# Kernel tuning notes

Hardware: AMD Instinct MI355X
Metric: run time of the kernel (lower is better)

Reference implementation:

```python
import jax, jax.numpy as jnp
import numpy as np

N_NODES = 50000
N_EDGES = 800000
D_IN = 64
D_OUT = 64


def setup_inputs() -> dict:
    key = jax.random.key(0)
    k1, k2, k3 = jax.random.split(key, 3)
    x = jax.random.normal(k1, (N_NODES, D_IN), dtype=jnp.float32)
    edge_index = jax.random.randint(k2, (2, N_EDGES), 0, N_NODES, dtype=jnp.int64)
    W = jax.random.normal(k3, (D_IN, D_OUT), dtype=jnp.float32) / np.sqrt(D_IN)
    b = jnp.zeros((D_OUT,), dtype=jnp.float32)
    return {"x": x, "edge_index": edge_index, "W": W, "b": b}


def reference(x, edge_index, W, b):
    # GCNConv with default add_self_loops=True and symmetric normalization,
    # followed by ReLU (GCN_layer activation).
    N = x.shape[0]
    loop = jnp.arange(N, dtype=edge_index.dtype)
    row = jnp.concatenate([edge_index[0], loop])  # source nodes [E+N]
    col = jnp.concatenate([edge_index[1], loop])  # target nodes [E+N]

    # degree of target nodes (includes self-loops)
    deg = jax.ops.segment_sum(jnp.ones_like(col, dtype=x.dtype), col, num_segments=N)
    deg_inv_sqrt = jnp.where(deg > 0, jax.lax.rsqrt(jnp.maximum(deg, 1.0)), 0.0)
    norm = deg_inv_sqrt[row] * deg_inv_sqrt[col]  # [E+N]

    xw = x @ W  # [N, Dout] - linear before propagation (as in PyG GCNConv)
    msg = norm[:, None] * xw[row]  # gather + per-edge scale, [E+N, Dout]
    out = jax.ops.segment_sum(msg, col, num_segments=N) + b  # scatter-add
    return jax.nn.relu(out)
```

## Files before the change

### kernel.cpp

```cpp
#include <hip/hip_runtime.h>

#define N_NODES 50000
#define N_EDGES 800000
#define D 64
#define CAP 64
#define NBLK_MM (N_NODES / 16)
#define NBLK_DEG (N_EDGES / 256)

typedef _Float16 half4_t __attribute__((ext_vector_type(4)));
typedef _Float16 half8_t __attribute__((ext_vector_type(8)));

__global__ __launch_bounds__(256) void k_mm_degbucket(const float* __restrict__ x,
                                                      const float* __restrict__ W,
                                                      _Float16* __restrict__ xwh,
                                                      const int* __restrict__ ei,
                                                      int* __restrict__ deg,
                                                      int* __restrict__ ebuf) {
    __shared__ float Wl[D * D];
    __shared__ float xl[16 * D];
    int bid = blockIdx.x >> 1;
    if (blockIdx.x & 1) {
        int e = bid * 256 + threadIdx.x;
        int r = ei[e];
        int c = ei[N_EDGES + e];
        int k = atomicAdd(&deg[c], 1);
        ebuf[(c << 6) | k] = r;
        return;
    }
    int tid = threadIdx.x;
#pragma unroll
    for (int i = tid; i < D * D / 4; i += 256)
        ((float4*)Wl)[i] = ((const float4*)W)[i];
    int r0 = bid * 16;
    ((float4*)xl)[tid] = ((const float4*)(x + (size_t)r0 * D))[tid];
    __syncthreads();
    int c4 = tid & 15;
    int rs = tid >> 4;
    const float* xrow = &xl[rs * D];
    const float* wc   = &Wl[c4 * 4];
    float acc0 = 0.f, acc1 = 0.f, acc2 = 0.f, acc3 = 0.f;
#pragma unroll
    for (int k4 = 0; k4 < 16; ++k4) {
        float4 xv = *(const float4*)(xrow + k4 * 4);
        float4 w0 = *(const float4*)(wc + (k4 * 4 + 0) * D);
        float4 w1 = *(const float4*)(wc + (k4 * 4 + 1) * D);
        float4 w2 = *(const float4*)(wc + (k4 * 4 + 2) * D);
        float4 w3 = *(const float4*)(wc + (k4 * 4 + 3) * D);
        acc0 = fmaf(xv.x, w0.x, fmaf(xv.y, w1.x, fmaf(xv.z, w2.x, fmaf(xv.w, w3.x, acc0))));
        acc1 = fmaf(xv.x, w0.y, fmaf(xv.y, w1.y, fmaf(xv.z, w2.y, fmaf(xv.w, w3.y, acc1))));
        acc2 = fmaf(xv.x, w0.z, fmaf(xv.y, w1.z, fmaf(xv.z, w2.z, fmaf(xv.w, w3.z, acc2))));
        acc3 = fmaf(xv.x, w0.w, fmaf(xv.y, w1.w, fmaf(xv.z, w2.w, fmaf(xv.w, w3.w, acc3))));
    }
    half4_t h = { (_Float16)acc0, (_Float16)acc1, (_Float16)acc2, (_Float16)acc3 };
    *(half4_t*)(xwh + (size_t)(r0 + rs) * D + c4 * 4) = h;
}

__global__ __launch_bounds__(256) void k_gather(const int* __restrict__ deg,
                                                const int* __restrict__ ebuf,
                                                const _Float16* __restrict__ xwh,
                                                const float* __restrict__ b,
                                                float* __restrict__ out) {
    int node = blockIdx.x * 4 + (threadIdx.x >> 6);
    int lane = threadIdx.x & 63;
    int g  = lane >> 3;
    int c8 = lane & 7;
    int cnt = deg[node];
    const int* eb = ebuf + ((size_t)node << 6);
    float acc[8] = {0.f, 0.f, 0.f, 0.f, 0.f, 0.f, 0.f, 0.f};
    for (int j = g; j < cnt; j += 8) {
        int r = eb[j];
        int d = deg[r];
        half8_t v = *(const half8_t*)(xwh + (size_t)r * D + c8 * 8);
        float s = rsqrtf((float)(d + 1));
#pragma unroll
        for (int i = 0; i < 8; ++i) acc[i] = fmaf(s, (float)v[i], acc[i]);
    }
#pragma unroll
    for (int m = 8; m <= 32; m <<= 1)
#pragma unroll
        for (int i = 0; i < 8; ++i) acc[i] += __shfl_xor(acc[i], m, 64);
    if (g == 0) {
        float dc = rsqrtf((float)(cnt + 1));
        half8_t xv = *(const half8_t*)(xwh + (size_t)node * D + c8 * 8);
        float4 b0 = *(const float4*)(b + c8 * 8);
        float4 b1 = *(const float4*)(b + c8 * 8 + 4);
        float o[8];
#pragma unroll
        for (int i = 0; i < 8; ++i)
            o[i] = dc * fmaf(dc, (float)xv[i], acc[i]);
        o[0] += b0.x; o[1] += b0.y; o[2] += b0.z; o[3] += b0.w;
        o[4] += b1.x; o[5] += b1.y; o[6] += b1.z; o[7] += b1.w;
#pragma unroll
        for (int i = 0; i < 8; ++i) o[i] = o[i] > 0.f ? o[i] : 0.f;
        float4 v0 = {o[0], o[1], o[2], o[3]};
        float4 v1 = {o[4], o[5], o[6], o[7]};
        *(float4*)(out + (size_t)node * D + c8 * 8)     = v0;
        *(float4*)(out + (size_t)node * D + c8 * 8 + 4) = v1;
    }
}

extern "C" void kernel_launch(void* const* d_in, const int* in_sizes, int n_in,
                              void* d_out, int out_size, void* d_ws, size_t ws_size,
                              hipStream_t stream) {
    const float* x  = (const float*)d_in[0];
    const int*   ei = (const int*)d_in[1];
    const float* W  = (const float*)d_in[2];
    const float* b  = (const float*)d_in[3];
    float* out = (float*)d_out;

    char* ws = (char*)d_ws;
    size_t off = 0;
    _Float16* xwh = (_Float16*)(ws + off); off += (size_t)N_NODES * D * sizeof(_Float16);
    int*   deg    = (int*)  (ws + off); off += (size_t)N_NODES * sizeof(int);
    int*   ebuf   = (int*)  (ws + off); off += (size_t)N_NODES * CAP * sizeof(int);

    hipMemsetAsync(deg, 0, (size_t)N_NODES * sizeof(int), stream);

    k_mm_degbucket<<<NBLK_MM + NBLK_DEG, 256, 0, stream>>>(x, W, xwh, ei, deg, ebuf);
    k_gather<<<N_NODES / 4, 256, 0, stream>>>(deg, ebuf, xwh, b, out);
}
```

Baseline: 135.2 us.

## Pad degree counters to 64-byte stride and precompute inverse-sqrt degrees

```diff
diff --git a/kernel.cpp b/kernel.cpp
--- a/kernel.cpp
+++ b/kernel.cpp
@@ -4,6 +4,7 @@
 #define N_EDGES 800000
 #define D 64
 #define CAP 64
+#define PAD 16
 #define NBLK_MM (N_NODES / 16)
 #define NBLK_DEG (N_EDGES / 256)
 
@@ -14,7 +15,7 @@
                                                       const float* __restrict__ W,
                                                       _Float16* __restrict__ xwh,
                                                       const int* __restrict__ ei,
-                                                      int* __restrict__ deg,
+                                                      int* __restrict__ deg16,
                                                       int* __restrict__ ebuf) {
     __shared__ float Wl[D * D];
     __shared__ float xl[16 * D];
@@ -23,7 +24,7 @@
         int e = bid * 256 + threadIdx.x;
         int r = ei[e];
         int c = ei[N_EDGES + e];
-        int k = atomicAdd(&deg[c], 1);
+        int k = atomicAdd(&deg16[c * PAD], 1);
         ebuf[(c << 6) | k] = r;
         return;
     }
@@ -55,7 +56,14 @@
     *(half4_t*)(xwh + (size_t)(r0 + rs) * D + c4 * 4) = h;
 }
 
-__global__ __launch_bounds__(256) void k_gather(const int* __restrict__ deg,
+__global__ __launch_bounds__(256) void k_dis(const int* __restrict__ deg16,
+                                             float* __restrict__ dis) {
+    int i = blockIdx.x * 256 + threadIdx.x;
+    if (i < N_NODES) dis[i] = rsqrtf((float)(deg16[i * PAD] + 1));
+}
+
+__global__ __launch_bounds__(256) void k_gather(const int* __restrict__ deg16,
+                                                const float* __restrict__ dis,
                                                 const int* __restrict__ ebuf,
                                                 const _Float16* __restrict__ xwh,
                                                 const float* __restrict__ b,
@@ -64,14 +72,13 @@
     int lane = threadIdx.x & 63;
     int g  = lane >> 3;
     int c8 = lane & 7;
-    int cnt = deg[node];
+    int cnt = deg16[node * PAD];
     const int* eb = ebuf + ((size_t)node << 6);
     float acc[8] = {0.f, 0.f, 0.f, 0.f, 0.f, 0.f, 0.f, 0.f};
     for (int j = g; j < cnt; j += 8) {
         int r = eb[j];
-        int d = deg[r];
+        float s = dis[r];
         half8_t v = *(const half8_t*)(xwh + (size_t)r * D + c8 * 8);
-        float s = rsqrtf((float)(d + 1));
 #pragma unroll
         for (int i = 0; i < 8; ++i) acc[i] = fmaf(s, (float)v[i], acc[i]);
     }
@@ -80,7 +87,7 @@
 #pragma unroll
         for (int i = 0; i < 8; ++i) acc[i] += __shfl_xor(acc[i], m, 64);
     if (g == 0) {
-        float dc = rsqrtf((float)(cnt + 1));
+        float dc = dis[node];
         half8_t xv = *(const half8_t*)(xwh + (size_t)node * D + c8 * 8);
         float4 b0 = *(const float4*)(b + c8 * 8);
         float4 b1 = *(const float4*)(b + c8 * 8 + 4);
@@ -111,11 +118,13 @@
     char* ws = (char*)d_ws;
     size_t off = 0;
     _Float16* xwh = (_Float16*)(ws + off); off += (size_t)N_NODES * D * sizeof(_Float16);
-    int*   deg    = (int*)  (ws + off); off += (size_t)N_NODES * sizeof(int);
+    int*   deg16  = (int*)  (ws + off); off += (size_t)N_NODES * PAD * sizeof(int);
+    float* dis    = (float*)(ws + off); off += (size_t)N_NODES * sizeof(float);
     int*   ebuf   = (int*)  (ws + off); off += (size_t)N_NODES * CAP * sizeof(int);
 
-    hipMemsetAsync(deg, 0, (size_t)N_NODES * sizeof(int), stream);
+    hipMemsetAsync(deg16, 0, (size_t)N_NODES * PAD * sizeof(int), stream);
 
-    k_mm_degbucket<<<NBLK_MM + NBLK_DEG, 256, 0, stream>>>(x, W, xwh, ei, deg, ebuf);
-    k_gather<<<N_NODES / 4, 256, 0, stream>>>(deg, ebuf, xwh, b, out);
+    k_mm_degbucket<<<NBLK_MM + NBLK_DEG, 256, 0, stream>>>(x, W, xwh, ei, deg16, ebuf);
+    k_dis<<<(N_NODES + 255) / 256, 256, 0, stream>>>(deg16, dis);
+    k_gather<<<N_NODES / 4, 256, 0, stream>>>(deg16, dis, ebuf, xwh, b, out);
 }
```

Measured after the change: 134.7 us. No clear change (-0.4%).
